# Kernel tuning notes

Hardware: AMD Instinct MI355X
Metric: run time of the kernel (lower is better)

## Reference

```python
import jax, jax.numpy as jnp
import numpy as np

B, S, E, H = 2, 2048, 768, 12
D = E // H  # head_dim = 64
EPS = 1e-5


def layernorm(x, g, b):
    mu = jnp.mean(x, axis=-1, keepdims=True)
    var = jnp.mean(jnp.square(x - mu), axis=-1, keepdims=True)
    return (x - mu) * jax.lax.rsqrt(var + EPS) * g + b


def setup_inputs() -> dict:
    key = jax.random.key(0)
    ks = jax.random.split(key, 8)
    std = 0.02
    return {
        "x": jax.random.normal(ks[0], (B, S, E), dtype=jnp.float32),
        "ln1_g": jnp.ones((E,), jnp.float32),
        "ln1_b": jnp.zeros((E,), jnp.float32),
        "w_attn": jax.random.normal(ks[1], (E, 3 * E), jnp.float32) * std,
        "b_attn": jnp.zeros((3 * E,), jnp.float32),
        "w_aproj": jax.random.normal(ks[2], (E, E), jnp.float32) * std,
        "b_aproj": jnp.zeros((E,), jnp.float32),
        "ln2_g": jnp.ones((E,), jnp.float32),
        "ln2_b": jnp.zeros((E,), jnp.float32),
        "w_fc": jax.random.normal(ks[3], (E, 4 * E), jnp.float32) * std,
        "b_fc": jnp.zeros((4 * E,), jnp.float32),
        "w_fproj": jax.random.normal(ks[4], (4 * E, E), jnp.float32) * std,
        "b_fproj": jnp.zeros((E,), jnp.float32),
    }


def reference(x, ln1_g, ln1_b, w_attn, b_attn, w_aproj, b_aproj,
              ln2_g, ln2_b, w_fc, b_fc, w_fproj, b_fproj):
    # --- attention sub-block (pre-LN) ---
    residual = x
    h = layernorm(x, ln1_g, ln1_b)
    qkv = h @ w_attn + b_attn                      # [B,S,3E]
    q, k, v = jnp.split(qkv, 3, axis=-1)
    # split heads -> [B,H,S,D]
    q = q.reshape(B, S, H, D).transpose(0, 2, 1, 3)
    k = k.reshape(B, S, H, D).transpose(0, 2, 1, 3)
    v = v.reshape(B, S, H, D).transpose(0, 2, 1, 3)
    # NOTE: original module applies NO 1/sqrt(D) scaling
    scores = jnp.einsum('bhqd,bhkd->bhqk', q, k)   # [B,H,S,S]
    causal = jnp.tril(jnp.ones((S, S), dtype=bool))
    mask_val = jnp.finfo(scores.dtype).min
    scores = jnp.where(causal, scores, mask_val)
    attn = jax.nn.softmax(scores, axis=-1)          # dropout = identity (eval)
    out = jnp.einsum('bhqk,bhkd->bhqd', attn, v)   # [B,H,S,D]
    out = out.transpose(0, 2, 1, 3).reshape(B, S, E)
    out = out @ w_aproj + b_aproj
    x = residual + out
    # --- MLP sub-block (pre-LN) ---
    residual = x
    h = layernorm(x, ln2_g, ln2_b)
    h = h @ w_fc + b_fc
    h = jax.nn.gelu(h, approximate=False)          # nn.GELU() exact erf form
    h = h @ w_fproj + b_fproj
    return residual + h
```

## Files before the change

kernel.cpp:

```cpp
#include <hip/hip_runtime.h>
#include <math.h>

#define B_ 2
#define S_ 2048
#define E_ 768
#define H_ 12
#define D_ 64
#define M_TOT (B_*S_)

typedef __attribute__((ext_vector_type(8))) short s16x8;
typedef __attribute__((ext_vector_type(4))) float f32x4;

__device__ __forceinline__ unsigned short f2bf(float f) {
  union { float f; unsigned u; } v; v.f = f;
  unsigned r = (v.u + 0x7fffu + ((v.u >> 16) & 1u)) >> 16;
  return (unsigned short)r;
}

__device__ __forceinline__ int swz(int r) { return ((r >> 3) ^ r) & 7; }

__device__ __forceinline__ void gload_lds16(const unsigned short* g, unsigned short* l) {
  __builtin_amdgcn_global_load_lds(
      (const __attribute__((address_space(1))) void*)g,
      (__attribute__((address_space(3))) void*)l, 16, 0, 0);
}

__global__ __launch_bounds__(256) void tconv_kernel(const float* __restrict__ in,
                                                    unsigned short* __restrict__ out,
                                                    int R, int C) {
  __shared__ float tile[32][33];
  int c0 = blockIdx.x * 32, r0 = blockIdx.y * 32;
  int t = threadIdx.x;
  int cl = t & 31, rl = t >> 5;
  #pragma unroll
  for (int p = 0; p < 4; ++p)
    tile[rl + p*8][cl] = in[(size_t)(r0 + rl + p*8)*C + c0 + cl];
  __syncthreads();
  int rl2 = t & 31, cl2 = t >> 5;
  #pragma unroll
  for (int p = 0; p < 4; ++p)
    out[(size_t)(c0 + cl2 + p*8)*R + r0 + rl2] = f2bf(tile[rl2][cl2 + p*8]);
}

__global__ __launch_bounds__(256) void vtrans_kernel(const unsigned short* __restrict__ qkv,
                                                     unsigned short* __restrict__ vt) {
  __shared__ unsigned short tile[32][33];
  int s0 = blockIdx.x * 32;
  int by = blockIdx.y;
  int bh = by >> 1, dh = by & 1;
  int b = bh / H_, h = bh % H_;
  int t = threadIdx.x;
  const unsigned short* src = qkv + (size_t)(b*S_)*2304 + 2*E_ + h*64 + dh*32;
  int srow = t >> 3, dq = t & 7;
  ushort4 v = *reinterpret_cast<const ushort4*>(src + (size_t)(s0 + srow)*2304 + dq*4);
  tile[srow][dq*4+0] = v.x; tile[srow][dq*4+1] = v.y;
  tile[srow][dq*4+2] = v.z; tile[srow][dq*4+3] = v.w;
  __syncthreads();
  int drow = t >> 3, sq = t & 7;
  ushort4 o;
  o.x = tile[sq*4+0][drow]; o.y = tile[sq*4+1][drow];
  o.z = tile[sq*4+2][drow]; o.w = tile[sq*4+3][drow];
  *reinterpret_cast<ushort4*>(vt + (size_t)(bh*64 + dh*32 + drow)*S_ + s0 + sq*4) = o;
}

__global__ __launch_bounds__(64) void ln_kernel(const float* __restrict__ x,
                                                const float* __restrict__ g,
                                                const float* __restrict__ b,
                                                unsigned short* __restrict__ out) {
  int row = blockIdx.x;
  int lane = threadIdx.x;
  const float* xr = x + (size_t)row * E_;
  float4 v[3];
  float s = 0.f, sq = 0.f;
  #pragma unroll
  for (int p = 0; p < 3; ++p) {
    v[p] = *reinterpret_cast<const float4*>(xr + p*256 + lane*4);
    s  += v[p].x + v[p].y + v[p].z + v[p].w;
    sq += v[p].x*v[p].x + v[p].y*v[p].y + v[p].z*v[p].z + v[p].w*v[p].w;
  }
  #pragma unroll
  for (int off = 32; off; off >>= 1) {
    s  += __shfl_xor(s,  off, 64);
    sq += __shfl_xor(sq, off, 64);
  }
  float mu  = s * (1.f/E_);
  float var = sq * (1.f/E_) - mu*mu;
  float rstd = rsqrtf(var + 1e-5f);
  unsigned short* orow = out + (size_t)row * E_;
  #pragma unroll
  for (int p = 0; p < 3; ++p) {
    int c = p*256 + lane*4;
    float4 gg = *reinterpret_cast<const float4*>(g + c);
    float4 bb = *reinterpret_cast<const float4*>(b + c);
    ushort4 o;
    o.x = f2bf((v[p].x-mu)*rstd*gg.x + bb.x);
    o.y = f2bf((v[p].y-mu)*rstd*gg.y + bb.y);
    o.z = f2bf((v[p].z-mu)*rstd*gg.z + bb.z);
    o.w = f2bf((v[p].w-mu)*rstd*gg.w + bb.w);
    *reinterpret_cast<ushort4*>(orow + c) = o;
  }
}

template<int MODE, int BM>
__global__ __launch_bounds__(256) void gemm_kernel(
    const unsigned short* __restrict__ A,
    const unsigned short* __restrict__ Wt,
    const float* __restrict__ bias,
    const float* __restrict__ res,
    unsigned short* __restrict__ outb,
    float* __restrict__ outf,
    int M, int N, int K)
{
  constexpr int Mi = BM / 32;
  constexpr int Ni = 4;
  __shared__ __align__(16) unsigned short As[BM*128];
  __shared__ __align__(16) unsigned short Ws[128*128];
  int n0 = blockIdx.x * 128, m0 = blockIdx.y * BM;
  int t = threadIdx.x, lane = t & 63, w = t >> 6;
  f32x4 acc[Mi][Ni] = {};
  int KT = K >> 7;

  auto stage = [&](int kt) {
    int k0 = kt << 7;
    #pragma unroll
    for (int p = 0; p < BM/16; ++p) {
      int off = p*2048 + w*512 + lane*8;
      int r = off >> 7;
      int slot = (off & 127) >> 3;
      int k8 = slot ^ swz(r);
      gload_lds16(A + (size_t)(m0 + r)*K + k0 + k8*8, As + p*2048 + w*512);
    }
    #pragma unroll
    for (int p = 0; p < 8; ++p) {
      int off = p*2048 + w*512 + lane*8;
      int r = off >> 7;
      int slot = (off & 127) >> 3;
      int k8 = slot ^ swz(r);
      gload_lds16(Wt + (size_t)(n0 + r)*K + k0 + k8*8, Ws + p*2048 + w*512);
    }
  };

  int wm = (w >> 1) * (BM/2), wn = (w & 1) * 64;
  int li = lane & 15, g = lane >> 4;

  int aoff[Mi], boff[Ni];
  #pragma unroll
  for (int mi = 0; mi < Mi; ++mi) {
    int r = wm + mi*16 + li;
    aoff[mi] = r*128 + ((g ^ swz(r)) << 3);
  }
  #pragma unroll
  for (int ni = 0; ni < Ni; ++ni) {
    int r = wn + ni*16 + li;
    boff[ni] = r*128 + ((g ^ swz(r)) << 3);
  }

  stage(0);
  for (int kt = 0; kt < KT; ++kt) {
    __syncthreads();
    #pragma unroll
    for (int kk = 0; kk < 4; ++kk) {
      int kx = kk << 5;
      s16x8 af[Mi], bf[Ni];
      #pragma unroll
      for (int mi = 0; mi < Mi; ++mi)
        af[mi] = *reinterpret_cast<const s16x8*>(As + (aoff[mi] ^ kx));
      #pragma unroll
      for (int ni = 0; ni < Ni; ++ni)
        bf[ni] = *reinterpret_cast<const s16x8*>(Ws + (boff[ni] ^ kx));
      #pragma unroll
      for (int mi = 0; mi < Mi; ++mi)
        #pragma unroll
        for (int ni = 0; ni < Ni; ++ni)
          acc[mi][ni] = __builtin_amdgcn_mfma_f32_16x16x32_bf16(af[mi], bf[ni], acc[mi][ni], 0, 0, 0);
    }
    __syncthreads();
    if (kt + 1 < KT) stage(kt + 1);
  }

  #pragma unroll
  for (int mi = 0; mi < Mi; ++mi) {
    #pragma unroll
    for (int j = 0; j < 4; ++j) {
      int row = m0 + wm + mi*16 + g*4 + j;
      #pragma unroll
      for (int ni = 0; ni < Ni; ++ni) {
        int col = n0 + wn + ni*16 + li;
        float v = acc[mi][ni][j] + bias[col];
        size_t idx = (size_t)row * N + col;
        if (MODE == 0) {
          outb[idx] = f2bf(v);
        } else if (MODE == 1) {
          outf[idx] = v + res[idx];
        } else {
          float gv = 0.5f * v * (1.f + erff(v * 0.70710678118f));
          outb[idx] = f2bf(gv);
        }
      }
    }
  }
}

__global__ __launch_bounds__(256) void attn_kernel(const unsigned short* __restrict__ qkv,
                                                   const unsigned short* __restrict__ vtg,
                                                   unsigned short* __restrict__ out,
                                                   float* __restrict__ part) {
  __shared__ __align__(16) unsigned short Ks[2][64*64];
  __shared__ __align__(16) unsigned short Vs[2][64*64];
  __shared__ __align__(16) unsigned short Pl[4][16*64];

  int gid = blockIdx.x;
  int bh = gid / 80, zi = gid % 80;
  int qt, ch;
  if (zi < 8)       { qt = zi;                ch = 0; }
  else if (zi < 24) { qt = 8  + ((zi-8)>>1);  ch = (zi-8) & 1; }
  else if (zi < 48) { qt = 16 + (zi-24)/3;    ch = (zi-24) % 3; }
  else              { qt = 24 + ((zi-48)>>2); ch = (zi-48) & 3; }
  int nc = (qt + 8) >> 3;
  int b = bh / H_, h = bh % H_;
  int t = threadIdx.x, lane = t & 63, w = t >> 6;
  int li = lane & 15, g = lane >> 4;
  const size_t rs = 3*E_;
  const unsigned short* base  = qkv + (size_t)b * S_ * rs;
  const unsigned short* kbase = base + E_ + h*64;
  const unsigned short* vbase = vtg + (size_t)bh * 64 * S_;

  int q0w = qt*64 + w*16;
  int qmin = q0w;
  s16x8 qf[2];
  #pragma unroll
  for (int f = 0; f < 2; ++f)
    qf[f] = *reinterpret_cast<const s16x8*>(base + (size_t)(q0w + li)*rs + h*64 + f*32 + g*8);

  float mrun = -1e30f, lrun = 0.f;
  f32x4 o[4] = {};

  auto stage = [&](int kvt, int buf) {
    int kv0 = kvt * 64;
    #pragma unroll
    for (int p = 0; p < 2; ++p) {
      int off = p*2048 + w*512 + lane*8;
      int r = off >> 6;
      int slot = (off & 63) >> 3;
      gload_lds16(kbase + (size_t)(kv0 + r)*rs + ((slot ^ (r & 7)) << 3),
                  &Ks[buf][p*2048 + w*512]);
      gload_lds16(vbase + (size_t)r*S_ + kv0 + ((slot ^ (r & 7)) << 3),
                  &Vs[buf][p*2048 + w*512]);
    }
  };

  int t0 = (ch * 512) >> 6;
  int t1 = min((ch + 1) * 512, (qt + 1) * 64) >> 6;

  stage(t0, 0);
  __syncthreads();

  for (int kt = t0; kt < t1; ++kt) {
    int cur = (kt - t0) & 1;
    if (kt + 1 < t1) stage(kt + 1, cur ^ 1);
    int kv0 = kt * 64;

    if (kv0 <= qmin + 15) {
      f32x4 pm[4];
      #pragma unroll
      for (int nh = 0; nh < 4; ++nh) {
        int r = nh*16 + li;
        int sw = r & 7;
        s16x8 kf0 = *reinterpret_cast<const s16x8*>(&Ks[cur][r*64 + ((g       ^ sw) << 3)]);
        s16x8 kf1 = *reinterpret_cast<const s16x8*>(&Ks[cur][r*64 + (((4 + g) ^ sw) << 3)]);
        f32x4 z = {};
        z = __builtin_amdgcn_mfma_f32_16x16x32_bf16(kf0, qf[0], z, 0, 0, 0);
        z = __builtin_amdgcn_mfma_f32_16x16x32_bf16(kf1, qf[1], z, 0, 0, 0);
        pm[nh] = z;
      }

      if (kv0 + 63 > qmin) {
        int q = qmin + li;
        #pragma unroll
        for (int nh = 0; nh < 4; ++nh)
          #pragma unroll
          for (int j = 0; j < 4; ++j) {
            int k = kv0 + nh*16 + g*4 + j;
            pm[nh][j] = (k <= q) ? pm[nh][j] : -1e30f;
          }
      }

      float tm = -1e30f;
      #pragma unroll
      for (int nh = 0; nh < 4; ++nh)
        tm = fmaxf(tm, fmaxf(fmaxf(pm[nh][0], pm[nh][1]), fmaxf(pm[nh][2], pm[nh][3])));
      tm = fmaxf(tm, __shfl_xor(tm, 16, 64));
      tm = fmaxf(tm, __shfl_xor(tm, 32, 64));
      float mnew = fmaxf(mrun, tm);
      float sc = __expf(mrun - mnew);
      mrun = mnew;

      unsigned short* Pw = Pl[w];
      float ps = 0.f;
      #pragma unroll
      for (int nh = 0; nh < 4; ++nh) {
        #pragma unroll
        for (int j = 0; j < 4; ++j) { pm[nh][j] = __expf(pm[nh][j] - mnew); ps += pm[nh][j]; }
        uint2 pk;
        pk.x = (unsigned)f2bf(pm[nh][0]) | ((unsigned)f2bf(pm[nh][1]) << 16);
        pk.y = (unsigned)f2bf(pm[nh][2]) | ((unsigned)f2bf(pm[nh][3]) << 16);
        int slot = 2*nh + (g >> 1);
        *reinterpret_cast<uint2*>(Pw + li*64 + ((slot ^ (li & 7)) << 3) + (g & 1)*4) = pk;
      }
      ps += __shfl_xor(ps, 16, 64);
      ps += __shfl_xor(ps, 32, 64);
      lrun = lrun*sc + ps;

      float scr[4];
      #pragma unroll
      for (int j = 0; j < 4; ++j) scr[j] = __shfl(sc, g*4 + j, 64);
      #pragma unroll
      for (int nc2 = 0; nc2 < 4; ++nc2)
        #pragma unroll
        for (int j = 0; j < 4; ++j) o[nc2][j] *= scr[j];

      asm volatile("s_waitcnt lgkmcnt(0)" ::: "memory");
      __builtin_amdgcn_sched_barrier(0);

      #pragma unroll
      for (int kk = 0; kk < 2; ++kk) {
        s16x8 pf = *reinterpret_cast<const s16x8*>(Pw + li*64 + (((kk*4 + g) ^ (li & 7)) << 3));
        #pragma unroll
        for (int nc2 = 0; nc2 < 4; ++nc2) {
          int r = nc2*16 + li;
          s16x8 vf = *reinterpret_cast<const s16x8*>(&Vs[cur][r*64 + (((kk*4 + g) ^ (r & 7)) << 3)]);
          o[nc2] = __builtin_amdgcn_mfma_f32_16x16x32_bf16(pf, vf, o[nc2], 0, 0, 0);
        }
      }
    }
    __syncthreads();
  }

  if (nc == 1) {
    float linv = 1.f / lrun;
    float lj[4];
    #pragma unroll
    for (int j = 0; j < 4; ++j) lj[j] = __shfl(linv, g*4 + j, 64);
    #pragma unroll
    for (int nc2 = 0; nc2 < 4; ++nc2)
      #pragma unroll
      for (int j = 0; j < 4; ++j)
        out[(size_t)(b*S_ + q0w + g*4 + j)*E_ + h*64 + nc2*16 + li] = f2bf(o[nc2][j] * lj[j]);
  } else {
    int cumP = (qt < 16) ? (qt-8)*2 : (qt < 24) ? 16 + (qt-16)*3 : 40 + (qt-24)*4;
    float* ps_ = part + (size_t)(bh*72 + cumP + ch) * 4224;
    #pragma unroll
    for (int nc2 = 0; nc2 < 4; ++nc2)
      #pragma unroll
      for (int j = 0; j < 4; ++j)
        ps_[(w*16 + g*4 + j)*64 + nc2*16 + li] = o[nc2][j];
    if (g == 0) {
      ps_[4096 + w*16 + li] = mrun;
      ps_[4160 + w*16 + li] = lrun;
    }
  }
}

__global__ __launch_bounds__(256) void merge_kernel(const float* __restrict__ part,
                                                    unsigned short* __restrict__ out) {
  int qt = 8 + blockIdx.x;
  int bh = blockIdx.y;
  int b = bh / H_, h = bh % H_;
  int t = threadIdx.x;
  int r = t >> 2, dg = (t & 3) * 16;
  int nc = (qt + 8) >> 3;
  int cumP = (qt < 16) ? (qt-8)*2 : (qt < 24) ? 16 + (qt-16)*3 : 40 + (qt-24)*4;
  const float* base = part + (size_t)(bh*72 + cumP) * 4224;

  float mv[4], lv[4];
  float M = -1e30f;
  for (int c = 0; c < nc; ++c) {
    mv[c] = base[c*4224 + 4096 + r];
    lv[c] = base[c*4224 + 4160 + r];
    M = fmaxf(M, mv[c]);
  }
  float wv[4], L = 0.f;
  for (int c = 0; c < nc; ++c) {
    wv[c] = __expf(mv[c] - M);
    L += lv[c] * wv[c];
  }
  float inv = 1.f / L;
  float acc[16] = {};
  for (int c = 0; c < nc; ++c) {
    const float* oc = base + c*4224 + r*64 + dg;
    #pragma unroll
    for (int j = 0; j < 16; j += 4) {
      float4 v = *reinterpret_cast<const float4*>(oc + j);
      acc[j+0] += v.x * wv[c];
      acc[j+1] += v.y * wv[c];
      acc[j+2] += v.z * wv[c];
      acc[j+3] += v.w * wv[c];
    }
  }
  unsigned short* orow = out + (size_t)(b*S_ + qt*64 + r)*E_ + h*64 + dg;
  ushort4 o4;
  #pragma unroll
  for (int j = 0; j < 16; j += 4) {
    o4.x = f2bf(acc[j+0]*inv); o4.y = f2bf(acc[j+1]*inv);
    o4.z = f2bf(acc[j+2]*inv); o4.w = f2bf(acc[j+3]*inv);
    *reinterpret_cast<ushort4*>(orow + j) = o4;
  }
}

extern "C" void kernel_launch(void* const* d_in, const int* in_sizes, int n_in,
                              void* d_out, int out_size, void* d_ws, size_t ws_size,
                              hipStream_t stream) {
  const float* x       = (const float*)d_in[0];
  const float* ln1g    = (const float*)d_in[1];
  const float* ln1b    = (const float*)d_in[2];
  const float* w_attn  = (const float*)d_in[3];
  const float* b_attn  = (const float*)d_in[4];
  const float* w_aproj = (const float*)d_in[5];
  const float* b_aproj = (const float*)d_in[6];
  const float* ln2g    = (const float*)d_in[7];
  const float* ln2b    = (const float*)d_in[8];
  const float* w_fc    = (const float*)d_in[9];
  const float* b_fc    = (const float*)d_in[10];
  const float* w_fproj = (const float*)d_in[11];
  const float* b_fproj = (const float*)d_in[12];
  float* out = (float*)d_out;

  char* ws = (char*)d_ws;
  unsigned short* h1       = (unsigned short*)(ws + 0);
  unsigned short* qkv      = (unsigned short*)(ws + 6291456);
  unsigned short* attno    = (unsigned short*)(ws + 25165824);
  float*          x2       = (float*)(ws + 31457280);
  unsigned short* h2       = (unsigned short*)(ws + 44040192);
  unsigned short* h3       = (unsigned short*)(ws + 50331648);
  unsigned short* wt_attn  = (unsigned short*)(ws + 75497472);
  unsigned short* wt_aproj = (unsigned short*)(ws + 79036416);
  unsigned short* wt_fc    = (unsigned short*)(ws + 80216064);
  unsigned short* wt_fproj = (unsigned short*)(ws + 84934656);
  unsigned short* vtg      = (unsigned short*)(ws + 89653248);
  float*          apart    = (float*)(ws + 44040192);

  tconv_kernel<<<dim3(2304/32,  768/32), 256, 0, stream>>>(w_attn,  wt_attn,  768, 2304);
  tconv_kernel<<<dim3( 768/32,  768/32), 256, 0, stream>>>(w_aproj, wt_aproj, 768,  768);
  tconv_kernel<<<dim3(3072/32,  768/32), 256, 0, stream>>>(w_fc,    wt_fc,    768, 3072);
  tconv_kernel<<<dim3( 768/32, 3072/32), 256, 0, stream>>>(w_fproj, wt_fproj, 3072, 768);

  ln_kernel<<<dim3(M_TOT), dim3(64), 0, stream>>>(x, ln1g, ln1b, h1);
  gemm_kernel<0,64><<<dim3(2304/128, M_TOT/64), 256, 0, stream>>>(h1, wt_attn, b_attn, nullptr, qkv, nullptr, M_TOT, 2304, 768);
  vtrans_kernel<<<dim3(S_/32, B_*H_*2), 256, 0, stream>>>(qkv, vtg);
  attn_kernel<<<dim3(24*80), dim3(256), 0, stream>>>(qkv, vtg, attno, apart);
  merge_kernel<<<dim3(24, 24), dim3(256), 0, stream>>>(apart, attno);
  gemm_kernel<1,64><<<dim3(768/128, M_TOT/64), 256, 0, stream>>>(attno, wt_aproj, b_aproj, x, nullptr, x2, M_TOT, 768, 768);
  ln_kernel<<<dim3(M_TOT), dim3(64), 0, stream>>>(x2, ln2g, ln2b, h2);
  gemm_kernel<2,64><<<dim3(3072/128, M_TOT/64), 256, 0, stream>>>(h2, wt_fc, b_fc, nullptr, h3, nullptr, M_TOT, 3072, 768);
  gemm_kernel<1,64><<<dim3(768/128, M_TOT/64), 256, 0, stream>>>(h3, wt_fproj, b_fproj, x2, nullptr, out, M_TOT, 768, 3072);
}
```

Before: 197.3 us.

## Double attention query tile to 128 rows per block for K/V reuse

The attention kernel now processes 128 query rows per block, with each wave handling two 16-row sub-blocks. Every staged K/V tile is therefore reused across twice as many queries, which halves global K/V traffic and the block count. The split-KV partition table, partial buffer layout and merge kernel are rescaled to match. It also precomputes LDS offsets, uses a packed bf16 conversion intrinsic and adds s_setprio around the MFMA sections. The cost is more registers per wave and fewer blocks, which may hurt occupancy and load balance.

```diff
diff --git a/kernel.cpp b/kernel.cpp
--- a/kernel.cpp
+++ b/kernel.cpp
@@ -1,4 +1,5 @@
 #include <hip/hip_runtime.h>
+#include <hip/hip_bf16.h>
 #include <math.h>
 
 #define B_ 2
@@ -15,6 +16,13 @@
   union { float f; unsigned u; } v; v.f = f;
   unsigned r = (v.u + 0x7fffu + ((v.u >> 16) & 1u)) >> 16;
   return (unsigned short)r;
+}
+
+__device__ __forceinline__ unsigned pkbf(float a, float b) {
+  __hip_bfloat162 h = __float22bfloat162_rn(make_float2(a, b));
+  unsigned u;
+  __builtin_memcpy(&u, &h, 4);
+  return u;
 }
 
 __device__ __forceinline__ int swz(int r) { return ((r >> 3) ^ r) & 7; }
@@ -207,16 +215,19 @@
                                                    float* __restrict__ part) {
   __shared__ __align__(16) unsigned short Ks[2][64*64];
   __shared__ __align__(16) unsigned short Vs[2][64*64];
-  __shared__ __align__(16) unsigned short Pl[4][16*64];
+  __shared__ __align__(16) unsigned short Pl[4][2][16*64];
 
   int gid = blockIdx.x;
-  int bh = gid / 80, zi = gid % 80;
+  int bh = gid / 40, zi = gid % 40;
   int qt, ch;
-  if (zi < 8)       { qt = zi;                ch = 0; }
-  else if (zi < 24) { qt = 8  + ((zi-8)>>1);  ch = (zi-8) & 1; }
-  else if (zi < 48) { qt = 16 + (zi-24)/3;    ch = (zi-24) % 3; }
-  else              { qt = 24 + ((zi-48)>>2); ch = (zi-48) & 3; }
-  int nc = (qt + 8) >> 3;
+  if (zi < 4) { qt = zi; ch = 0; }
+  else {
+    int rem = zi - 4;
+    if (rem < 8)       { qt = 4  + (rem >> 1);       ch = rem & 1; }
+    else if (rem < 20) { qt = 8  + (rem - 8) / 3;    ch = (rem - 8) % 3; }
+    else               { qt = 12 + ((rem - 20) >> 2); ch = (rem - 20) & 3; }
+  }
+  int nc = (qt + 4) >> 2;
   int b = bh / H_, h = bh % H_;
   int t = threadIdx.x, lane = t & 63, w = t >> 6;
   int li = lane & 15, g = lane >> 4;
@@ -225,15 +236,35 @@
   const unsigned short* kbase = base + E_ + h*64;
   const unsigned short* vbase = vtg + (size_t)bh * 64 * S_;
 
-  int q0w = qt*64 + w*16;
-  int qmin = q0w;
-  s16x8 qf[2];
-  #pragma unroll
-  for (int f = 0; f < 2; ++f)
-    qf[f] = *reinterpret_cast<const s16x8*>(base + (size_t)(q0w + li)*rs + h*64 + f*32 + g*8);
-
-  float mrun = -1e30f, lrun = 0.f;
-  f32x4 o[4] = {};
+  int q0w = qt*128 + w*32;
+  s16x8 qf[2][2];
+  #pragma unroll
+  for (int rb = 0; rb < 2; ++rb)
+    #pragma unroll
+    for (int f = 0; f < 2; ++f)
+      qf[rb][f] = *reinterpret_cast<const s16x8*>(base + (size_t)(q0w + rb*16 + li)*rs + h*64 + f*32 + g*8);
+
+  int koff0[4], koff1[4], poff[4], prd[2], voff[2][4];
+  #pragma unroll
+  for (int nh = 0; nh < 4; ++nh) {
+    int r = nh*16 + li, sw_ = r & 7;
+    koff0[nh] = r*64 + ((g ^ sw_) << 3);
+    koff1[nh] = r*64 + (((4 + g) ^ sw_) << 3);
+    poff[nh]  = li*64 + (((2*nh + (g >> 1)) ^ (li & 7)) << 3) + (g & 1)*4;
+  }
+  #pragma unroll
+  for (int kk = 0; kk < 2; ++kk) {
+    prd[kk] = li*64 + (((kk*4 + g) ^ (li & 7)) << 3);
+    #pragma unroll
+    for (int n2 = 0; n2 < 4; ++n2) {
+      int r = n2*16 + li;
+      voff[kk][n2] = r*64 + (((kk*4 + g) ^ (r & 7)) << 3);
+    }
+  }
+
+  float mrun[2] = {-1e30f, -1e30f};
+  float lrun[2] = {0.f, 0.f};
+  f32x4 o[2][4] = {};
 
   auto stage = [&](int kvt, int buf) {
     int kv0 = kvt * 64;
@@ -250,7 +281,7 @@
   };
 
   int t0 = (ch * 512) >> 6;
-  int t1 = min((ch + 1) * 512, (qt + 1) * 64) >> 6;
+  int t1 = min((ch + 1) * 512, (qt + 1) * 128) >> 6;
 
   stage(t0, 0);
   __syncthreads();
@@ -260,19 +291,23 @@
     if (kt + 1 < t1) stage(kt + 1, cur ^ 1);
     int kv0 = kt * 64;
 
-    if (kv0 <= qmin + 15) {
+    #pragma unroll
+    for (int rb = 0; rb < 2; ++rb) {
+      int qmin = q0w + rb*16;
+      if (kv0 > qmin + 15) continue;
+
       f32x4 pm[4];
+      __builtin_amdgcn_s_setprio(1);
       #pragma unroll
       for (int nh = 0; nh < 4; ++nh) {
-        int r = nh*16 + li;
-        int sw = r & 7;
-        s16x8 kf0 = *reinterpret_cast<const s16x8*>(&Ks[cur][r*64 + ((g       ^ sw) << 3)]);
-        s16x8 kf1 = *reinterpret_cast<const s16x8*>(&Ks[cur][r*64 + (((4 + g) ^ sw) << 3)]);
+        s16x8 kf0 = *reinterpret_cast<const s16x8*>(&Ks[cur][koff0[nh]]);
+        s16x8 kf1 = *reinterpret_cast<const s16x8*>(&Ks[cur][koff1[nh]]);
         f32x4 z = {};
-        z = __builtin_amdgcn_mfma_f32_16x16x32_bf16(kf0, qf[0], z, 0, 0, 0);
-        z = __builtin_amdgcn_mfma_f32_16x16x32_bf16(kf1, qf[1], z, 0, 0, 0);
+        z = __builtin_amdgcn_mfma_f32_16x16x32_bf16(kf0, qf[rb][0], z, 0, 0, 0);
+        z = __builtin_amdgcn_mfma_f32_16x16x32_bf16(kf1, qf[rb][1], z, 0, 0, 0);
         pm[nh] = z;
       }
+      __builtin_amdgcn_s_setprio(0);
 
       if (kv0 + 63 > qmin) {
         int q = qmin + li;
@@ -291,92 +326,98 @@
         tm = fmaxf(tm, fmaxf(fmaxf(pm[nh][0], pm[nh][1]), fmaxf(pm[nh][2], pm[nh][3])));
       tm = fmaxf(tm, __shfl_xor(tm, 16, 64));
       tm = fmaxf(tm, __shfl_xor(tm, 32, 64));
-      float mnew = fmaxf(mrun, tm);
-      float sc = __expf(mrun - mnew);
-      mrun = mnew;
-
-      unsigned short* Pw = Pl[w];
+      float mnew = fmaxf(mrun[rb], tm);
+      float sc = __expf(mrun[rb] - mnew);
+      mrun[rb] = mnew;
+
+      unsigned short* Pw = Pl[w][rb];
       float ps = 0.f;
       #pragma unroll
       for (int nh = 0; nh < 4; ++nh) {
         #pragma unroll
         for (int j = 0; j < 4; ++j) { pm[nh][j] = __expf(pm[nh][j] - mnew); ps += pm[nh][j]; }
         uint2 pk;
-        pk.x = (unsigned)f2bf(pm[nh][0]) | ((unsigned)f2bf(pm[nh][1]) << 16);
-        pk.y = (unsigned)f2bf(pm[nh][2]) | ((unsigned)f2bf(pm[nh][3]) << 16);
-        int slot = 2*nh + (g >> 1);
-        *reinterpret_cast<uint2*>(Pw + li*64 + ((slot ^ (li & 7)) << 3) + (g & 1)*4) = pk;
+        pk.x = pkbf(pm[nh][0], pm[nh][1]);
+        pk.y = pkbf(pm[nh][2], pm[nh][3]);
+        *reinterpret_cast<uint2*>(Pw + poff[nh]) = pk;
       }
       ps += __shfl_xor(ps, 16, 64);
       ps += __shfl_xor(ps, 32, 64);
-      lrun = lrun*sc + ps;
+      lrun[rb] = lrun[rb]*sc + ps;
 
       float scr[4];
       #pragma unroll
       for (int j = 0; j < 4; ++j) scr[j] = __shfl(sc, g*4 + j, 64);
       #pragma unroll
-      for (int nc2 = 0; nc2 < 4; ++nc2)
-        #pragma unroll
-        for (int j = 0; j < 4; ++j) o[nc2][j] *= scr[j];
+      for (int n2 = 0; n2 < 4; ++n2)
+        #pragma unroll
+        for (int j = 0; j < 4; ++j) o[rb][n2][j] *= scr[j];
 
       asm volatile("s_waitcnt lgkmcnt(0)" ::: "memory");
       __builtin_amdgcn_sched_barrier(0);
 
+      __builtin_amdgcn_s_setprio(1);
       #pragma unroll
       for (int kk = 0; kk < 2; ++kk) {
-        s16x8 pf = *reinterpret_cast<const s16x8*>(Pw + li*64 + (((kk*4 + g) ^ (li & 7)) << 3));
-        #pragma unroll
-        for (int nc2 = 0; nc2 < 4; ++nc2) {
-          int r = nc2*16 + li;
-          s16x8 vf = *reinterpret_cast<const s16x8*>(&Vs[cur][r*64 + (((kk*4 + g) ^ (r & 7)) << 3)]);
-          o[nc2] = __builtin_amdgcn_mfma_f32_16x16x32_bf16(pf, vf, o[nc2], 0, 0, 0);
+        s16x8 pf = *reinterpret_cast<const s16x8*>(Pw + prd[kk]);
+        #pragma unroll
+        for (int n2 = 0; n2 < 4; ++n2) {
+          s16x8 vf = *reinterpret_cast<const s16x8*>(&Vs[cur][voff[kk][n2]]);
+          o[rb][n2] = __builtin_amdgcn_mfma_f32_16x16x32_bf16(pf, vf, o[rb][n2], 0, 0, 0);
         }
       }
+      __builtin_amdgcn_s_setprio(0);
     }
     __syncthreads();
   }
 
   if (nc == 1) {
-    float linv = 1.f / lrun;
-    float lj[4];
-    #pragma unroll
-    for (int j = 0; j < 4; ++j) lj[j] = __shfl(linv, g*4 + j, 64);
-    #pragma unroll
-    for (int nc2 = 0; nc2 < 4; ++nc2)
-      #pragma unroll
-      for (int j = 0; j < 4; ++j)
-        out[(size_t)(b*S_ + q0w + g*4 + j)*E_ + h*64 + nc2*16 + li] = f2bf(o[nc2][j] * lj[j]);
+    #pragma unroll
+    for (int rb = 0; rb < 2; ++rb) {
+      float linv = 1.f / lrun[rb];
+      float lj[4];
+      #pragma unroll
+      for (int j = 0; j < 4; ++j) lj[j] = __shfl(linv, g*4 + j, 64);
+      #pragma unroll
+      for (int n2 = 0; n2 < 4; ++n2)
+        #pragma unroll
+        for (int j = 0; j < 4; ++j)
+          out[(size_t)(b*S_ + q0w + rb*16 + g*4 + j)*E_ + h*64 + n2*16 + li] = f2bf(o[rb][n2][j] * lj[j]);
+    }
   } else {
-    int cumP = (qt < 16) ? (qt-8)*2 : (qt < 24) ? 16 + (qt-16)*3 : 40 + (qt-24)*4;
-    float* ps_ = part + (size_t)(bh*72 + cumP + ch) * 4224;
-    #pragma unroll
-    for (int nc2 = 0; nc2 < 4; ++nc2)
-      #pragma unroll
-      for (int j = 0; j < 4; ++j)
-        ps_[(w*16 + g*4 + j)*64 + nc2*16 + li] = o[nc2][j];
-    if (g == 0) {
-      ps_[4096 + w*16 + li] = mrun;
-      ps_[4160 + w*16 + li] = lrun;
+    int cumP = (qt < 8) ? (qt-4)*2 : (qt < 12) ? 8 + (qt-8)*3 : 20 + (qt-12)*4;
+    float* ps_ = part + (size_t)(bh*36 + cumP + ch) * 8448;
+    #pragma unroll
+    for (int rb = 0; rb < 2; ++rb) {
+      #pragma unroll
+      for (int n2 = 0; n2 < 4; ++n2)
+        #pragma unroll
+        for (int j = 0; j < 4; ++j)
+          ps_[(w*32 + rb*16 + g*4 + j)*64 + n2*16 + li] = o[rb][n2][j];
+      if (g == 0) {
+        ps_[8192 + w*32 + rb*16 + li] = mrun[rb];
+        ps_[8320 + w*32 + rb*16 + li] = lrun[rb];
+      }
     }
   }
 }
 
 __global__ __launch_bounds__(256) void merge_kernel(const float* __restrict__ part,
                                                     unsigned short* __restrict__ out) {
-  int qt = 8 + blockIdx.x;
+  int qt = 4 + blockIdx.x;
   int bh = blockIdx.y;
   int b = bh / H_, h = bh % H_;
   int t = threadIdx.x;
-  int r = t >> 2, dg = (t & 3) * 16;
-  int nc = (qt + 8) >> 3;
-  int cumP = (qt < 16) ? (qt-8)*2 : (qt < 24) ? 16 + (qt-16)*3 : 40 + (qt-24)*4;
-  const float* base = part + (size_t)(bh*72 + cumP) * 4224;
+  int r = t >> 1, dg = (t & 1) * 32;
+  int nc = (qt + 4) >> 2;
+  int cumP = (qt < 8) ? (qt-4)*2 : (qt < 12) ? 8 + (qt-8)*3 : 20 + (qt-12)*4;
+  const float* base = part + (size_t)(bh*36 + cumP) * 8448;
 
   float mv[4], lv[4];
   float M = -1e30f;
   for (int c = 0; c < nc; ++c) {
-    mv[c] = base[c*4224 + 4096 + r];
-    lv[c] = base[c*4224 + 4160 + r];
+    mv[c] = base[c*8448 + 8192 + r];
+    lv[c] = base[c*8448 + 8320 + r];
     M = fmaxf(M, mv[c]);
   }
   float wv[4], L = 0.f;
@@ -385,11 +426,11 @@
     L += lv[c] * wv[c];
   }
   float inv = 1.f / L;
-  float acc[16] = {};
+  float acc[32] = {};
   for (int c = 0; c < nc; ++c) {
-    const float* oc = base + c*4224 + r*64 + dg;
-    #pragma unroll
-    for (int j = 0; j < 16; j += 4) {
+    const float* oc = base + c*8448 + r*64 + dg;
+    #pragma unroll
+    for (int j = 0; j < 32; j += 4) {
       float4 v = *reinterpret_cast<const float4*>(oc + j);
       acc[j+0] += v.x * wv[c];
       acc[j+1] += v.y * wv[c];
@@ -397,10 +438,10 @@
       acc[j+3] += v.w * wv[c];
     }
   }
-  unsigned short* orow = out + (size_t)(b*S_ + qt*64 + r)*E_ + h*64 + dg;
+  unsigned short* orow = out + (size_t)(b*S_ + qt*128 + r)*E_ + h*64 + dg;
   ushort4 o4;
   #pragma unroll
-  for (int j = 0; j < 16; j += 4) {
+  for (int j = 0; j < 32; j += 4) {
     o4.x = f2bf(acc[j+0]*inv); o4.y = f2bf(acc[j+1]*inv);
     o4.z = f2bf(acc[j+2]*inv); o4.w = f2bf(acc[j+3]*inv);
     *reinterpret_cast<ushort4*>(orow + j) = o4;
@@ -447,8 +488,8 @@
   ln_kernel<<<dim3(M_TOT), dim3(64), 0, stream>>>(x, ln1g, ln1b, h1);
   gemm_kernel<0,64><<<dim3(2304/128, M_TOT/64), 256, 0, stream>>>(h1, wt_attn, b_attn, nullptr, qkv, nullptr, M_TOT, 2304, 768);
   vtrans_kernel<<<dim3(S_/32, B_*H_*2), 256, 0, stream>>>(qkv, vtg);
-  attn_kernel<<<dim3(24*80), dim3(256), 0, stream>>>(qkv, vtg, attno, apart);
-  merge_kernel<<<dim3(24, 24), dim3(256), 0, stream>>>(apart, attno);
+  attn_kernel<<<dim3(24*40), dim3(256), 0, stream>>>(qkv, vtg, attno, apart);
+  merge_kernel<<<dim3(12, 24), dim3(256), 0, stream>>>(apart, attno);
   gemm_kernel<1,64><<<dim3(768/128, M_TOT/64), 256, 0, stream>>>(attno, wt_aproj, b_aproj, x, nullptr, x2, M_TOT, 768, 768);
   ln_kernel<<<dim3(M_TOT), dim3(64), 0, stream>>>(x2, ln2g, ln2b, h2);
   gemm_kernel<2,64><<<dim3(3072/128, M_TOT/64), 256, 0, stream>>>(h2, wt_fc, b_fc, nullptr, h3, nullptr, M_TOT, 3072, 768);
```

Result: slower. 208.0 us (+5.5%).
